# Kernel optimization log

Hardware: AMD Instinct MI355X
Metric: run time of the kernel (lower is better)

The kernel has to match this reference:

```python
import jax, jax.numpy as jnp
import numpy as np

B, N, TOP_K = 4, 2048, 30
NUM_PE, NUM_RBF, EDGE_F = 16, 16, 128

def l2norm(x, eps=1e-12):
    return x / jnp.maximum(jnp.linalg.norm(x, axis=-1, keepdims=True), eps)

def gather_nodes(nodes, idx):
    # nodes [B,N,C], idx [B,N,K] -> [B,N,K,C]
    return jax.vmap(lambda n, i: n[i])(nodes, idx)

def setup_inputs() -> dict:
    key = jax.random.key(0)
    k1, k2 = jax.random.split(key)
    X = jax.random.normal(k1, (B, N, 3), dtype=jnp.float32) * 5.0
    mask = jnp.ones((B, N), dtype=jnp.float32)
    W = jax.random.normal(k2, (NUM_PE + NUM_RBF + 7, EDGE_F), dtype=jnp.float32) * 0.1
    b = jnp.zeros((EDGE_F,), dtype=jnp.float32)
    gamma = jnp.ones((EDGE_F,), dtype=jnp.float32)
    beta = jnp.zeros((EDGE_F,), dtype=jnp.float32)
    return {"X": X, "mask": mask, "W": W, "b": b, "gamma": gamma, "beta": beta}

def _quaternions(R):
    # R [B,N,K,3,3] -> Q [B,N,K,4]
    diag = jnp.diagonal(R, axis1=-2, axis2=-1)  # [B,N,K,3]
    Rxx, Ryy, Rzz = diag[..., 0], diag[..., 1], diag[..., 2]
    mags = 0.5 * jnp.sqrt(jnp.abs(1.0 + jnp.stack(
        [Rxx - Ryy - Rzz, -Rxx + Ryy - Rzz, -Rxx - Ryy + Rzz], -1)))
    signs = jnp.sign(jnp.stack([
        R[..., 2, 1] - R[..., 1, 2],
        R[..., 0, 2] - R[..., 2, 0],
        R[..., 1, 0] - R[..., 0, 1]], -1))
    xyz = signs * mags
    w = jnp.sqrt(jax.nn.relu(1.0 + jnp.sum(diag, -1, keepdims=True))) / 2.0
    Q = jnp.concatenate((xyz, w), -1)
    return l2norm(Q)

def _forward(X, mask, W, b, gamma, beta):
    eps = 1e-6
    # pairwise distances + top-k neighbors
    mask_2D = mask[:, None, :] * mask[:, :, None]
    dXp = X[:, None, :, :] - X[:, :, None, :]
    D = mask_2D * jnp.sqrt(jnp.sum(dXp ** 2, -1) + eps)
    D_max = jnp.max(D, -1, keepdims=True)
    D_adjust = D + (1.0 - mask_2D) * D_max
    neg_vals, E_idx = jax.lax.top_k(-D_adjust, TOP_K)
    D_neighbors = -neg_vals

    # RBF
    D_mu = jnp.linspace(0.0, 20.0, NUM_RBF)
    D_sigma = 20.0 / NUM_RBF
    RBF = jnp.exp(-(((D_neighbors[..., None] - D_mu) / D_sigma) ** 2))

    # orientations
    dX = X[:, 1:, :] - X[:, :-1, :]
    U = l2norm(dX)
    u_2, u_1 = U[:, :-2, :], U[:, 1:-1, :]
    n_2 = l2norm(jnp.cross(u_2, u_1))
    o_1 = l2norm(u_2 - u_1)
    O = jnp.stack((o_1, n_2, jnp.cross(o_1, n_2)), 2)  # [B,N-3,3,3]
    O9 = O.reshape(O.shape[0], O.shape[1], 9)
    O9 = jnp.pad(O9, ((0, 0), (1, 2), (0, 0)))  # [B,N,9]
    O_neighbors = gather_nodes(O9, E_idx).reshape(B, N, TOP_K, 3, 3)
    X_neighbors = gather_nodes(X, E_idx)  # [B,N,K,3]
    Om = O9.reshape(B, N, 3, 3)
    dXn = X_neighbors - X[:, :, None, :]
    dU = l2norm(jnp.einsum('bnij,bnkj->bnki', Om, dXn))
    R = jnp.einsum('bnji,bnkjl->bnkil', Om, O_neighbors)
    Q = _quaternions(R)
    O_features = jnp.concatenate((dU, Q), -1)  # [B,N,K,7]

    # positional encodings
    ii = jnp.arange(N, dtype=jnp.float32)[None, :, None]
    d = (E_idx.astype(jnp.float32) - ii)[..., None]
    freq = jnp.exp(jnp.arange(0, NUM_PE, 2, dtype=jnp.float32) * -(np.log(10000.0) / NUM_PE))
    angles = d * freq
    E_positional = jnp.concatenate((jnp.cos(angles), jnp.sin(angles)), -1)

    E = jnp.concatenate((E_positional, RBF, O_features), -1)  # [B,N,K,39]
    E = E @ W + b
    # Normalize (LayerNorm w/ unbiased std, as in struct2seq Normalize)
    mu = jnp.mean(E, -1, keepdims=True)
    sigma = jnp.sqrt(jnp.var(E, -1, keepdims=True, ddof=1) + eps)
    E = gamma * (E - mu) / (sigma + eps) + beta
    return E, E_idx

def reference(X, mask, W, b, gamma, beta):
    return _forward(X, mask, W, b, gamma, beta)
```

## Files before the change

### kernel.cpp

```cpp
#include <hip/hip_runtime.h>
#include <stdint.h>

#define B_ 4
#define N_ 2048
#define K_ 30
#define F_ 128
#define NF 39

typedef unsigned long long u64;
typedef float f32x4 __attribute__((ext_vector_type(4)));
typedef short s16x8 __attribute__((ext_vector_type(8)));

__device__ __forceinline__ u64 umin64(u64 a, u64 b) { return a < b ? a : b; }

template <int CTRL>
__device__ __forceinline__ float dpp_add(float x) {
    int r = __builtin_amdgcn_update_dpp(0, __float_as_int(x), CTRL, 0xF, 0xF, true);
    return x + __int_as_float(r);
}
__device__ __forceinline__ float rowsum16(float x) {
    x = dpp_add<0xB1>(x);
    x = dpp_add<0x4E>(x);
    x = dpp_add<0x141>(x);
    x = dpp_add<0x140>(x);
    return x;
}

__device__ __forceinline__ unsigned int bf16rne(float f) {
    unsigned int u = __float_as_uint(f);
    return (u + 0x7FFFu + ((u >> 16) & 1u)) >> 16;
}
__device__ __forceinline__ unsigned int bfpack(float a, float b) {
    return bf16rne(a) | (bf16rne(b) << 16);
}

__global__ __launch_bounds__(256) void topk_kernel(const float* __restrict__ X,
                                                   float* __restrict__ O9,
                                                   int* __restrict__ Eidx,
                                                   float* __restrict__ Dn,
                                                   float* __restrict__ EidxF) {
    __shared__ float xs[N_], ys[N_], zs[N_];
    __shared__ u64 surv[4][64];
    int t = threadIdx.x, lane = t & 63, wid = t >> 6;
    int node = blockIdx.x * 4 + wid;
    int i = node & (N_ - 1);
    const float* Xb = X + (size_t)(node - i) * 3;

    for (int idx = t; idx < 3 * N_; idx += 256) {
        float v = Xb[idx];
        int j = idx / 3, c = idx - 3 * j;
        if (c == 0) xs[j] = v; else if (c == 1) ys[j] = v; else zs[j] = v;
    }
    __syncthreads();

    if (t < 4) {
        int nn = blockIdx.x * 4 + t;
        int ii = nn & (N_ - 1);
        float o[9] = {0.f,0.f,0.f,0.f,0.f,0.f,0.f,0.f,0.f};
        if (ii >= 1 && ii <= N_ - 3) {
            float ax = xs[ii-1], ay = ys[ii-1], az = zs[ii-1];
            float bx = xs[ii],   by = ys[ii],   bz = zs[ii];
            float cx = xs[ii+1], cy = ys[ii+1], cz = zs[ii+1];
            float u2x = bx-ax, u2y = by-ay, u2z = bz-az;
            float n2_ = sqrtf(u2x*u2x+u2y*u2y+u2z*u2z);
            float inv = 1.0f / fmaxf(n2_, 1e-12f);
            u2x*=inv; u2y*=inv; u2z*=inv;
            float u1x = cx-bx, u1y = cy-by, u1z = cz-bz;
            float n1_ = sqrtf(u1x*u1x+u1y*u1y+u1z*u1z);
            inv = 1.0f / fmaxf(n1_, 1e-12f);
            u1x*=inv; u1y*=inv; u1z*=inv;
            float nx = u2y*u1z - u2z*u1y;
            float ny = u2z*u1x - u2x*u1z;
            float nz = u2x*u1y - u2y*u1x;
            float nn2 = sqrtf(nx*nx+ny*ny+nz*nz);
            inv = 1.0f / fmaxf(nn2, 1e-12f);
            nx*=inv; ny*=inv; nz*=inv;
            float ox = u2x-u1x, oy = u2y-u1y, oz = u2z-u1z;
            float no = sqrtf(ox*ox+oy*oy+oz*oz);
            inv = 1.0f / fmaxf(no, 1e-12f);
            ox*=inv; oy*=inv; oz*=inv;
            o[0]=ox; o[1]=oy; o[2]=oz;
            o[3]=nx; o[4]=ny; o[5]=nz;
            o[6]=oy*nz - oz*ny; o[7]=oz*nx - ox*nz; o[8]=ox*ny - oy*nx;
        }
        float* dst = O9 + (size_t)nn * 9;
        #pragma unroll
        for (int q = 0; q < 9; ++q) dst[q] = o[q];
    }

    float xi = xs[i], yi = ys[i], zi = zs[i];

    unsigned int d[32];
    #pragma unroll
    for (int s = 0; s < 32; ++s) {
        int j = lane + (s << 6);
        float dx = __fsub_rn(xs[j], xi);
        float dy = __fsub_rn(ys[j], yi);
        float dz = __fsub_rn(zs[j], zi);
        float s1 = __fadd_rn(__fmul_rn(dx,dx), __fmul_rn(dy,dy));
        float s2 = __fadd_rn(s1, __fmul_rn(dz,dz));
        d[s] = __float_as_uint(__fadd_rn(s2, 1e-6f));
    }

    unsigned int lm = d[0];
    #pragma unroll
    for (int s = 1; s < 32; ++s) lm = min(lm, d[s]);

    unsigned int v32 = lm;
    #pragma unroll
    for (int k = 2; k <= 64; k <<= 1) {
        #pragma unroll
        for (int j = k >> 1; j >= 1; j >>= 1) {
            unsigned int o = (unsigned int)__shfl_xor((int)v32, j, 64);
            bool up = ((lane & k) == 0);
            bool lower = ((lane & j) == 0);
            v32 = (lower == up) ? min(v32, o) : max(v32, o);
        }
    }
    unsigned int Bcut = (unsigned int)__shfl((int)v32, K_ - 1, 64) + 64u;

    int base = 0;
    #pragma unroll
    for (int s = 0; s < 32; ++s) {
        bool p = (d[s] <= Bcut);
        u64 blt = __ballot(p);
        if (p) {
            int slot = base + (int)__popcll(blt & ((1ull << lane) - 1ull));
            if (slot < 64) {
                float D = __fsqrt_rn(__uint_as_float(d[s]));
                surv[wid][slot] = (((u64)__float_as_uint(D)) << 32)
                                | (unsigned int)(lane + (s << 6));
            }
        }
        base += (int)__popcll(blt);
    }
    int cnt = base;

    if (cnt <= 64) {
        if (lane == 0 && cnt < 64) surv[wid][cnt] = ~0ull;
        u64 my = surv[wid][lane];
        int rank = 0;
        for (int r = 0; r < cnt; r += 2) {
            ulonglong2 kk = *(const ulonglong2*)&surv[wid][r];
            rank += (kk.x < my) ? 1 : 0;
            rank += (kk.y < my) ? 1 : 0;
        }
        if (lane < cnt && rank < K_) {
            int j = (int)(my & 0xffffffffull);
            int o = node * K_ + rank;
            Eidx[o] = j;
            Dn[o] = __uint_as_float((unsigned int)(my >> 32));
            EidxF[o] = (float)j;
        }
    } else {
        #pragma unroll
        for (int s = 0; s < 32; ++s)
            d[s] = __float_as_uint(__fsqrt_rn(__uint_as_float(d[s])));
        for (int k = 0; k < K_; ++k) {
            u64 m = ~0ull;
            #pragma unroll
            for (int s = 0; s < 32; ++s) {
                u64 kk = (((u64)d[s]) << 32) | (unsigned int)(lane + (s << 6));
                m = umin64(m, kk);
            }
            #pragma unroll
            for (int off = 1; off < 64; off <<= 1)
                m = umin64(m, (u64)__shfl_xor((long long)m, off, 64));
            #pragma unroll
            for (int s = 0; s < 32; ++s) {
                u64 kk = (((u64)d[s]) << 32) | (unsigned int)(lane + (s << 6));
                if (kk == m) d[s] = 0xFFFFFFFFu;
            }
            if (lane == 0) {
                int o = node * K_ + k;
                int j = (int)(m & 0xffffffffull);
                Eidx[o] = j;
                Dn[o] = __uint_as_float((unsigned int)(m >> 32));
                EidxF[o] = (float)j;
            }
        }
    }
}

__global__ __launch_bounds__(256) void edge_fused(const float* __restrict__ X,
                                                  const float* __restrict__ O9,
                                                  const int* __restrict__ Eidx,
                                                  const float* __restrict__ Dn,
                                                  const float* __restrict__ W,
                                                  const float* __restrict__ bias,
                                                  const float* __restrict__ gamma,
                                                  const float* __restrict__ beta,
                                                  float* __restrict__ E) {
    __shared__ unsigned int ldsF[128 * 32];
    __shared__ unsigned int ldsW[128 * 32];
    int t = threadIdx.x, lane = t & 63, wid = t >> 6;
    int e0 = blockIdx.x * 128;

    if (t < 128) {
        int e = e0 + t;
        int b = e / (N_ * K_);
        int rem = e - b * (N_ * K_);
        int i = rem / K_;
        int node = b * N_ + i;
        int j = Eidx[e];
        float dnb = Dn[e];

        float f[40];
        float dd = (float)(j - i);
        const float freqs[8] = {1.0f, 0.31622776601683794f, 0.1f, 0.031622776601683794f,
                                0.01f, 0.0031622776601683794f, 0.001f, 0.00031622776601683794f};
        #pragma unroll
        for (int l = 0; l < 8; ++l) {
            float a = dd * freqs[l];
            float sv, cv;
            __sincosf(a, &sv, &cv);
            f[l] = cv;
            f[8 + l] = sv;
        }
        #pragma unroll
        for (int r = 0; r < 16; ++r) {
            float mu = (20.0f / 15.0f) * (float)r;
            float u = (dnb - mu) * 0.8f;
            f[16 + r] = __expf(-u * u);
        }
        const float* Omp = O9 + (size_t)node * 9;
        float Om[9];
        #pragma unroll
        for (int q = 0; q < 9; ++q) Om[q] = Omp[q];
        const float* Xi = X + (size_t)node * 3;
        const float* Xj = X + (size_t)(b * N_ + j) * 3;
        float dx = Xj[0] - Xi[0], dy = Xj[1] - Xi[1], dz = Xj[2] - Xi[2];
        float v0 = Om[0]*dx + Om[1]*dy + Om[2]*dz;
        float v1 = Om[3]*dx + Om[4]*dy + Om[5]*dz;
        float v2 = Om[6]*dx + Om[7]*dy + Om[8]*dz;
        float n = sqrtf(v0*v0 + v1*v1 + v2*v2);
        float inv = 1.0f / fmaxf(n, 1e-12f);
        f[32] = v0 * inv; f[33] = v1 * inv; f[34] = v2 * inv;
        const float* On = O9 + (size_t)(b * N_ + j) * 9;
        float R00 = Om[0]*On[0] + Om[3]*On[3] + Om[6]*On[6];
        float R01 = Om[0]*On[1] + Om[3]*On[4] + Om[6]*On[7];
        float R02 = Om[0]*On[2] + Om[3]*On[5] + Om[6]*On[8];
        float R10 = Om[1]*On[0] + Om[4]*On[3] + Om[7]*On[6];
        float R11 = Om[1]*On[1] + Om[4]*On[4] + Om[7]*On[7];
        float R12 = Om[1]*On[2] + Om[4]*On[5] + Om[7]*On[8];
        float R20 = Om[2]*On[0] + Om[5]*On[3] + Om[8]*On[6];
        float R21 = Om[2]*On[1] + Om[5]*On[4] + Om[8]*On[7];
        float R22 = Om[2]*On[2] + Om[5]*On[5] + Om[8]*On[8];
        float mg0 = 0.5f * sqrtf(fabsf(1.0f + R00 - R11 - R22));
        float mg1 = 0.5f * sqrtf(fabsf(1.0f - R00 + R11 - R22));
        float mg2 = 0.5f * sqrtf(fabsf(1.0f - R00 - R11 + R22));
        float t0 = R21 - R12, t1 = R02 - R20, t2 = R10 - R01;
        float s0 = (t0 > 0.f) ? 1.f : ((t0 < 0.f) ? -1.f : 0.f);
        float s1 = (t1 > 0.f) ? 1.f : ((t1 < 0.f) ? -1.f : 0.f);
        float s2 = (t2 > 0.f) ? 1.f : ((t2 < 0.f) ? -1.f : 0.f);
        float q0 = s0 * mg0, q1 = s1 * mg1, q2 = s2 * mg2;
        float w = sqrtf(fmaxf(1.0f + R00 + R11 + R22, 0.0f)) * 0.5f;
        float nq = sqrtf(q0*q0 + q1*q1 + q2*q2 + w*w);
        inv = 1.0f / fmaxf(nq, 1e-12f);
        f[35] = q0 * inv; f[36] = q1 * inv; f[37] = q2 * inv; f[38] = w * inv;
        f[39] = 0.0f;

        int row = t;
        #pragma unroll
        for (int c = 0; c < 8; ++c) {
            uint4 u;
            if (c < 5) {
                u.x = bfpack(f[8*c+0], f[8*c+1]);
                u.y = bfpack(f[8*c+2], f[8*c+3]);
                u.z = bfpack(f[8*c+4], f[8*c+5]);
                u.w = bfpack(f[8*c+6], f[8*c+7]);
            } else {
                u = make_uint4(0u, 0u, 0u, 0u);
            }
            int idx = row * 32 + ((4 * c) ^ ((row & 7) << 2));
            *(uint4*)&ldsF[idx] = u;
        }
    } else {
        int col = t - 128;
        #pragma unroll
        for (int c8 = 0; c8 < 8; ++c8) {
            uint4 u;
            unsigned int* up = (unsigned int*)&u;
            #pragma unroll
            for (int m = 0; m < 4; ++m) {
                int k0 = 8 * c8 + 2 * m, k1 = k0 + 1;
                float a  = (k0 < NF) ? W[k0 * F_ + col] : 0.f;
                float bv = (k1 < NF) ? W[k1 * F_ + col] : 0.f;
                up[m] = bfpack(a, bv);
            }
            int idx = col * 32 + ((4 * c8) ^ ((col & 7) << 2));
            *(uint4*)&ldsW[idx] = u;
        }
    }

    float gg[8], be8[8], bb[8];
    #pragma unroll
    for (int tt = 0; tt < 8; ++tt) {
        int c = 16 * tt + (lane & 15);
        gg[tt] = gamma[c]; be8[tt] = beta[c]; bb[tt] = bias[c];
    }

    __syncthreads();

    s16x8 wf[8][2];
    #pragma unroll
    for (int tt = 0; tt < 8; ++tt) {
        int col = 16 * tt + (lane & 15);
        #pragma unroll
        for (int s = 0; s < 2; ++s) {
            int idx = col * 32 + ((((lane >> 4) * 4) + s * 16) ^ ((col & 7) << 2));
            wf[tt][s] = *(s16x8*)&ldsW[idx];
        }
    }

    #pragma unroll
    for (int wt = 0; wt < 2; ++wt) {
        int ebase = wid * 32 + wt * 16;
        int arow = ebase + (lane & 15);
        s16x8 af[2];
        #pragma unroll
        for (int s = 0; s < 2; ++s) {
            int idx = arow * 32 + ((((lane >> 4) * 4) + s * 16) ^ ((arow & 7) << 2));
            af[s] = *(s16x8*)&ldsF[idx];
        }
        f32x4 acc[8];
        #pragma unroll
        for (int tt = 0; tt < 8; ++tt) {
            acc[tt] = (f32x4){0.f, 0.f, 0.f, 0.f};
            acc[tt] = __builtin_amdgcn_mfma_f32_16x16x32_bf16(af[0], wf[tt][0], acc[tt], 0, 0, 0);
            acc[tt] = __builtin_amdgcn_mfma_f32_16x16x32_bf16(af[1], wf[tt][1], acc[tt], 0, 0, 0);
        }
        float sum[4] = {0,0,0,0}, sq[4] = {0,0,0,0};
        #pragma unroll
        for (int tt = 0; tt < 8; ++tt) {
            #pragma unroll
            for (int q = 0; q < 4; ++q) {
                float v = acc[tt][q] + bb[tt];
                acc[tt][q] = v;
                sum[q] += v;
                sq[q] = fmaf(v, v, sq[q]);
            }
        }
        float muv[4], invv[4];
        #pragma unroll
        for (int q = 0; q < 4; ++q) {
            float S  = rowsum16(sum[q]);
            float Qs = rowsum16(sq[q]);
            float mu = S * (1.0f / 128.0f);
            float var = (Qs - S * mu) * (1.0f / 127.0f);
            muv[q] = mu;
            invv[q] = 1.0f / (sqrtf(var + 1e-6f) + 1e-6f);
        }
        size_t base = (size_t)(e0 + ebase) * F_;
        #pragma unroll
        for (int tt = 0; tt < 8; ++tt) {
            int c = 16 * tt + (lane & 15);
            #pragma unroll
            for (int q = 0; q < 4; ++q) {
                int er = (lane >> 4) * 4 + q;
                E[base + (size_t)er * F_ + c] =
                    gg[tt] * (acc[tt][q] - muv[q]) * invv[q] + be8[tt];
            }
        }
    }
}

extern "C" void kernel_launch(void* const* d_in, const int* in_sizes, int n_in,
                              void* d_out, int out_size, void* d_ws, size_t ws_size,
                              hipStream_t stream) {
    const float* X     = (const float*)d_in[0];
    const float* W     = (const float*)d_in[2];
    const float* bias  = (const float*)d_in[3];
    const float* gamma = (const float*)d_in[4];
    const float* beta  = (const float*)d_in[5];

    float* E      = (float*)d_out;
    float* EidxF  = (float*)d_out + (size_t)B_ * N_ * K_ * F_;

    float* O9   = (float*)d_ws;
    int*   Eidx = (int*)(O9 + (size_t)B_ * N_ * 9);
    float* Dn   = (float*)(Eidx + (size_t)B_ * N_ * K_);

    int nodes = B_ * N_;
    int edges = nodes * K_;

    hipLaunchKernelGGL(topk_kernel, dim3(nodes / 4), dim3(256), 0, stream,
                       X, O9, Eidx, Dn, EidxF);
    hipLaunchKernelGGL(edge_fused, dim3(edges / 128), dim3(256), 0, stream,
                       X, O9, Eidx, Dn, W, bias, gamma, beta, E);
}
```

Baseline: 51.26 us.

## Use float4 AoS shared coordinates and 8 nodes per topk block

Stores the batch's point coordinates in shared memory as float4 entries instead of three separate SoA arrays, so each distance evaluation does a single 128-bit LDS read. It also doubles the block to 512 threads handling 8 query nodes, which halves the number of times each batch's coordinates are loaded from global into LDS per node. The shared footprint grows to 32KB per block, and the launch bounds request 6 waves per SIMD, which may limit occupancy or registers.

```diff
diff --git a/kernel.cpp b/kernel.cpp
--- a/kernel.cpp
+++ b/kernel.cpp
@@ -34,38 +34,39 @@
     return bf16rne(a) | (bf16rne(b) << 16);
 }
 
-__global__ __launch_bounds__(256) void topk_kernel(const float* __restrict__ X,
-                                                   float* __restrict__ O9,
-                                                   int* __restrict__ Eidx,
-                                                   float* __restrict__ Dn,
-                                                   float* __restrict__ EidxF) {
-    __shared__ float xs[N_], ys[N_], zs[N_];
-    __shared__ u64 surv[4][64];
+__global__ __launch_bounds__(512, 6) void topk_kernel(const float* __restrict__ X,
+                                                      float* __restrict__ O9,
+                                                      int* __restrict__ Eidx,
+                                                      float* __restrict__ Dn,
+                                                      float* __restrict__ EidxF) {
+    __shared__ float4 P[N_];
+    __shared__ u64 surv[8][64];
     int t = threadIdx.x, lane = t & 63, wid = t >> 6;
-    int node = blockIdx.x * 4 + wid;
+    int node = blockIdx.x * 8 + wid;
     int i = node & (N_ - 1);
     const float* Xb = X + (size_t)(node - i) * 3;
-
-    for (int idx = t; idx < 3 * N_; idx += 256) {
+    float* Pf = (float*)P;
+
+    #pragma unroll
+    for (int r = 0; r < 12; ++r) {
+        int idx = t + r * 512;
         float v = Xb[idx];
         int j = idx / 3, c = idx - 3 * j;
-        if (c == 0) xs[j] = v; else if (c == 1) ys[j] = v; else zs[j] = v;
+        Pf[4 * j + c] = v;
     }
     __syncthreads();
 
-    if (t < 4) {
-        int nn = blockIdx.x * 4 + t;
+    if (t < 8) {
+        int nn = blockIdx.x * 8 + t;
         int ii = nn & (N_ - 1);
         float o[9] = {0.f,0.f,0.f,0.f,0.f,0.f,0.f,0.f,0.f};
         if (ii >= 1 && ii <= N_ - 3) {
-            float ax = xs[ii-1], ay = ys[ii-1], az = zs[ii-1];
-            float bx = xs[ii],   by = ys[ii],   bz = zs[ii];
-            float cx = xs[ii+1], cy = ys[ii+1], cz = zs[ii+1];
-            float u2x = bx-ax, u2y = by-ay, u2z = bz-az;
+            float4 A = P[ii-1], Bv = P[ii], C = P[ii+1];
+            float u2x = Bv.x-A.x, u2y = Bv.y-A.y, u2z = Bv.z-A.z;
             float n2_ = sqrtf(u2x*u2x+u2y*u2y+u2z*u2z);
             float inv = 1.0f / fmaxf(n2_, 1e-12f);
             u2x*=inv; u2y*=inv; u2z*=inv;
-            float u1x = cx-bx, u1y = cy-by, u1z = cz-bz;
+            float u1x = C.x-Bv.x, u1y = C.y-Bv.y, u1z = C.z-Bv.z;
             float n1_ = sqrtf(u1x*u1x+u1y*u1y+u1z*u1z);
             inv = 1.0f / fmaxf(n1_, 1e-12f);
             u1x*=inv; u1y*=inv; u1z*=inv;
@@ -88,15 +89,16 @@
         for (int q = 0; q < 9; ++q) dst[q] = o[q];
     }
 
-    float xi = xs[i], yi = ys[i], zi = zs[i];
+    float4 ci = P[i];
+    float xi = ci.x, yi = ci.y, zi = ci.z;
 
     unsigned int d[32];
     #pragma unroll
     for (int s = 0; s < 32; ++s) {
-        int j = lane + (s << 6);
-        float dx = __fsub_rn(xs[j], xi);
-        float dy = __fsub_rn(ys[j], yi);
-        float dz = __fsub_rn(zs[j], zi);
+        float4 p = P[lane + (s << 6)];
+        float dx = __fsub_rn(p.x, xi);
+        float dy = __fsub_rn(p.y, yi);
+        float dz = __fsub_rn(p.z, zi);
         float s1 = __fadd_rn(__fmul_rn(dx,dx), __fmul_rn(dy,dy));
         float s2 = __fadd_rn(s1, __fmul_rn(dz,dz));
         d[s] = __float_as_uint(__fadd_rn(s2, 1e-6f));
@@ -384,7 +386,7 @@
     int nodes = B_ * N_;
     int edges = nodes * K_;
 
-    hipLaunchKernelGGL(topk_kernel, dim3(nodes / 4), dim3(256), 0, stream,
+    hipLaunchKernelGGL(topk_kernel, dim3(nodes / 8), dim3(512), 0, stream,
                        X, O9, Eidx, Dn, EidxF);
     hipLaunchKernelGGL(edge_fused, dim3(edges / 128), dim3(256), 0, stream,
                        X, O9, Eidx, Dn, W, bias, gamma, beta, E);
```

New measurement: 47.07 us. 1.09x faster.
